# Kernel tuning notes

Hardware: AMD Instinct MI355X
Metric: run time of the kernel (lower is better)

Reference implementation:

```python
import jax, jax.numpy as jnp
import numpy as np

ZERO = 1e-8
L = 2            # num_gnn_layers
D = 256          # dim_node_features
B = 32           # graphs per batch
NPG = 256        # nodes per graph
N = B * NPG      # total nodes
E = 131072       # edges per edge-type
MAX_TOKENS = 256 # MAX_TOKENS_OF_A_POST
UPD = 0.5        # args.updated_weights_for_A


def _make_edges(k):
    k1, k2, k3 = jax.random.split(k, 3)
    g = jax.random.randint(k1, (E,), 0, B) * NPG          # keep edges within a graph
    src = g + jax.random.randint(k2, (E,), 0, NPG)
    dst = g + jax.random.randint(k3, (E,), 0, NPG)
    return jnp.stack([src, dst]).astype(jnp.int64)


def setup_inputs() -> dict:
    key = jax.random.key(0)
    ks = jax.random.split(key, 12)
    x = jax.random.normal(ks[0], (N, D), dtype=jnp.float32)
    ei_e = _make_edges(ks[1]); ew_e = jax.random.uniform(ks[2], (E,), dtype=jnp.float32)
    ei_p = _make_edges(ks[3]); ew_p = jax.random.uniform(ks[4], (E,), dtype=jnp.float32)
    ei_o = _make_edges(ks[5]); ew_o = jax.random.uniform(ks[6], (E,), dtype=jnp.float32)
    entity_mask = jax.random.randint(ks[7], (B, NPG), 0, 2).astype(bool)
    pattern_mask = jax.random.randint(ks[8], (B, NPG), 0, 2).astype(bool)
    s = 1.0 / np.sqrt(D)
    W_gcn = (jax.random.normal(ks[9], (L, 3, D, D), dtype=jnp.float32) * s)
    b_gcn = jnp.zeros((L, 3, D), dtype=jnp.float32)
    T_dyn = (jax.random.normal(ks[10], (L, D, D), dtype=jnp.float32) * s)
    return {
        'x': x,
        'edge_index_entity': ei_e, 'edge_weight_entity': ew_e,
        'edge_index_pattern': ei_p, 'edge_weight_pattern': ew_p,
        'edge_index_others': ei_o, 'edge_weight_others': ew_o,
        'entity_mask': entity_mask, 'pattern_mask': pattern_mask,
        'W_gcn': W_gcn, 'b_gcn': b_gcn, 'T_dyn': T_dyn,
    }


def _normalized_correlation_matrix(H):
    # cosine-similarity correlation matrix, symmetrically degree-normalized
    nrm = jnp.sqrt(jnp.sum(H * H, axis=1))
    A = (H @ H.T) / (nrm[:, None] * nrm[None, :] + ZERO)
    dinv = 1.0 / jnp.sqrt(jnp.abs(jnp.sum(A, axis=1)) + ZERO)
    return dinv[:, None] * A * dinv[None, :]


def _gcn(H, W, b, ei, ew):
    # GCNConv(add_self_loops=False, normalize=False): scatter-sum of weighted source messages
    msg = (H @ W)[ei[0]] * ew[:, None]                     # [E, D]
    return jax.ops.segment_sum(msg, ei[1], num_segments=N) + b


def _forward(x, we0, wp0, wo0, W_gcn, b_gcn, T_dyn,
             ei_e, ei_p, ei_o, entity_mask, pattern_mask):
    H = x
    A = _normalized_correlation_matrix(H)                  # [N, N]
    for i in range(L):
        if i == 0:
            we, wp, wo = we0, wp0, wo0
        else:
            # diag(one_hot(src) @ A @ one_hot(dst).T) == A[src, dst]
            we = A[ei_e[0], ei_e[1]]
            wp = A[ei_p[0], ei_p[1]]
            wo = A[ei_o[0], ei_o[1]]
        He = _gcn(H, W_gcn[i, 0], b_gcn[i, 0], ei_e, we)
        Hp = _gcn(H, W_gcn[i, 1], b_gcn[i, 1], ei_p, wp)
        Ho = _gcn(H, W_gcn[i, 2], b_gcn[i, 2], ei_o, wo)
        H = jax.nn.relu(He + Hp + Ho)
        A_hat = jax.nn.sigmoid((H @ T_dyn[i]) @ H.T)
        A = (1.0 - UPD) * A + UPD * A_hat
    # per-graph diagonal blocks of A  -> [B, NPG, NPG]
    A4 = A.reshape(B, NPG, B, NPG)
    idx = jnp.arange(B)
    blocks = A4[idx, :, idx, :]
    A_sum = jnp.sum(blocks, axis=-1)                       # [B, NPG]
    ent_cols = jnp.einsum('bij,bj->bi', blocks, entity_mask.astype(A.dtype))
    pat_cols = jnp.einsum('bij,bj->bi', blocks, pattern_mask.astype(A.dtype))
    map_pattern = A_sum - ent_cols
    map_entity = A_sum - pat_cols

    def finish(m):
        mn = jnp.min(m, axis=1, keepdims=True)
        mx = jnp.max(m, axis=1, keepdims=True)
        m = (m - mn) / (mx - mn + ZERO)
        m = m / (jnp.sum(m, axis=1, keepdims=True) + ZERO)
        return m[:, :MAX_TOKENS]                           # padding() with NPG==MAX_TOKENS

    return finish(map_entity), finish(map_pattern)


def reference(x, edge_index_entity, edge_weight_entity,
              edge_index_pattern, edge_weight_pattern,
              edge_index_others, edge_weight_others,
              entity_mask, pattern_mask, W_gcn, b_gcn, T_dyn):
    return _forward(x, edge_weight_entity, edge_weight_pattern, edge_weight_others,
                    W_gcn, b_gcn, T_dyn,
                    edge_index_entity, edge_index_pattern, edge_index_others,
                    entity_mask, pattern_mask)
```

## Files before the change

kernel.cpp:

```cpp
#include <hip/hip_runtime.h>

#define NND   8192
#define DDIM  256
#define NGRP  32
#define ZEROF 1e-8f
#define LSTR  40
#define TSTR  72
#define OFF_AH 0
#define OFF_AL 2560
#define OFF_BH 5120
#define OFF_BL 10240
#define OFF_TT 5120
#define LDS_U16 16384

typedef unsigned short u16;
typedef __attribute__((ext_vector_type(8))) short short8v;
typedef __attribute__((ext_vector_type(4))) float float4v;

__device__ inline u16 f2bf(float x) {
  unsigned u = __float_as_uint(x);
  u += 0x7fffu + ((u >> 16) & 1u);
  return (u16)(u >> 16);
}
__device__ inline float bf2f(u16 h) { return __uint_as_float((unsigned)h << 16); }
__device__ inline void split2(float x, u16& h, u16& l) {
  h = f2bf(x);
  l = f2bf(x - bf2f(h));
}

__device__ inline float wave_sum(float v) {
#pragma unroll
  for (int off = 32; off > 0; off >>= 1) v += __shfl_down(v, off, 64);
  return v;
}

#define LOAD_REGS(tt, kk)                                                                   \
  {                                                                                         \
    int m_ = tid >> 2, kq_ = (tid & 3) * 8;                                                 \
    size_t aoff_;                                                                           \
    if (MODE == 1)                                                                          \
      aoff_ = (size_t)((tt) * 256 + bym * 64 + m_) * 8192 + (size_t)(g * 256 + (kk) + kq_); \
    else if (MODE == 2 || MODE == 3)                                                        \
      aoff_ = (size_t)(g * 256 + bym * 64 + m_) * 256 + (kk) + kq_;                         \
    else                                                                                    \
      aoff_ = (size_t)(bym * 64 + m_) * 256 + (kk) + kq_;                                   \
    rAh = *(const short8v*)&Ah_g[aoff_];                                                    \
    rAl = *(const short8v*)&Al_g[aoff_];                                                    \
    size_t bbase_ = (MODE == 1) ? ((size_t)(g * 3 + (tt)) << 16)                            \
                  : ((MODE == 2 || MODE == 3) ? ((size_t)g << 16) : (size_t)0);             \
    if (HALF) {                                                                             \
      int n_ = tid & 63, kq2_ = (tid >> 6) * 8;                                             \
      size_t boff_ = bbase_ + (size_t)(col0 + n_) * 256 + (kk) + kq2_;                      \
      rBh0 = *(const short8v*)&Bh_g[boff_];                                                 \
      rBl0 = *(const short8v*)&Bl_g[boff_];                                                 \
    } else {                                                                                \
      int n_ = tid & 127, kq2_ = (tid >> 7) * 16;                                           \
      size_t boff_ = bbase_ + (size_t)(col0 + n_) * 256 + (kk) + kq2_;                      \
      rBh0 = *(const short8v*)&Bh_g[boff_]; rBh1 = *(const short8v*)&Bh_g[boff_ + 8];       \
      rBl0 = *(const short8v*)&Bl_g[boff_]; rBl1 = *(const short8v*)&Bl_g[boff_ + 8];       \
    }                                                                                       \
  }

template<int MODE, bool HALF>
__device__ __forceinline__ void mfma_body(
    u16* lds,
    const u16* __restrict__ Ah_g, const u16* __restrict__ Al_g,
    const u16* __restrict__ Bh_g, const u16* __restrict__ Bl_g,
    float* __restrict__ Cf, u16* __restrict__ Ch, u16* __restrict__ Cl,
    const float* __restrict__ nrm, const float* __restrict__ dinv,
    const float* __restrict__ bias,
    int bxm, int bym, int g) {
  u16* Ahs = lds + OFF_AH;
  u16* Als = lds + OFF_AL;
  u16* Bhs = lds + OFF_BH;
  u16* Bls = lds + OFF_BL;
  u16* Tt  = lds + OFF_TT;
  const int NJ = HALF ? 2 : 4;
  const int tid = threadIdx.x;
  const int col0 = bxm * (HALF ? 64 : 128);
  const int w = tid >> 6, lane = tid & 63;
  const int lm = lane & 15, lq = lane >> 4;
  const int wr = (w >> 1) * 32, wc = (w & 1) * (HALF ? 32 : 64);

  float4v acc[2][4];
#pragma unroll
  for (int i = 0; i < 2; ++i)
#pragma unroll
    for (int j = 0; j < NJ; ++j) acc[i][j] = (float4v)0.f;

  short8v rAh, rAl, rBh0, rBh1, rBl0, rBl1;
  const int TOTAL = (MODE == 1) ? 24 : 8;

  LOAD_REGS(0, 0);
  for (int step = 0; step < TOTAL; ++step) {
    if (step) __syncthreads();
    {
      int m = tid >> 2, kq = (tid & 3) * 8;
      *(short8v*)&Ahs[m * LSTR + kq] = rAh;
      *(short8v*)&Als[m * LSTR + kq] = rAl;
    }
    if (HALF) {
      int n = tid & 63, kq2 = (tid >> 6) * 8;
      *(short8v*)&Bhs[n * LSTR + kq2] = rBh0;
      *(short8v*)&Bls[n * LSTR + kq2] = rBl0;
    } else {
      int n = tid & 127, kq2 = (tid >> 7) * 16;
      *(short8v*)&Bhs[n * LSTR + kq2] = rBh0; *(short8v*)&Bhs[n * LSTR + kq2 + 8] = rBh1;
      *(short8v*)&Bls[n * LSTR + kq2] = rBl0; *(short8v*)&Bls[n * LSTR + kq2 + 8] = rBl1;
    }
    __syncthreads();
    int nxt = step + 1;
    if (nxt < TOTAL) {
      int tt = nxt >> 3, kk = (nxt & 7) * 32;
      LOAD_REGS(tt, kk);
    }
    short8v ah[2], al[2], bh[4], bl[4];
#pragma unroll
    for (int i = 0; i < 2; ++i) {
      int r = wr + i * 16 + lm;
      ah[i] = *(const short8v*)&Ahs[r * LSTR + lq * 8];
      al[i] = *(const short8v*)&Als[r * LSTR + lq * 8];
    }
#pragma unroll
    for (int j = 0; j < NJ; ++j) {
      int r = wc + j * 16 + lm;
      bh[j] = *(const short8v*)&Bhs[r * LSTR + lq * 8];
      bl[j] = *(const short8v*)&Bls[r * LSTR + lq * 8];
    }
#pragma unroll
    for (int i = 0; i < 2; ++i)
#pragma unroll
      for (int j = 0; j < NJ; ++j) {
        acc[i][j] = __builtin_amdgcn_mfma_f32_16x16x32_bf16(ah[i], bh[j], acc[i][j], 0, 0, 0);
        acc[i][j] = __builtin_amdgcn_mfma_f32_16x16x32_bf16(ah[i], bl[j], acc[i][j], 0, 0, 0);
        acc[i][j] = __builtin_amdgcn_mfma_f32_16x16x32_bf16(al[i], bh[j], acc[i][j], 0, 0, 0);
      }
  }

  if (MODE == 2 || MODE == 3) {
#pragma unroll
    for (int i = 0; i < 2; ++i) {
#pragma unroll
      for (int r = 0; r < 4; ++r) {
        int grow = g * 256 + bym * 64 + wr + i * 16 + lq * 4 + r;
        float di = 0.f, ni = 0.f;
        if (MODE == 2) { di = dinv[grow]; ni = nrm[grow]; }
#pragma unroll
        for (int j = 0; j < NJ; ++j) {
          int gcol = col0 + wc + j * 16 + lm;
          size_t ci = (size_t)grow * 256 + gcol;
          float v = acc[i][j][r];
          if (MODE == 2) {
            int gj = g * 256 + gcol;
            Cf[ci] = v * di * dinv[gj] / (ni * nrm[gj] + ZEROF);
          } else {
            Cf[ci] = 0.5f * Cf[ci] + 0.5f * (1.f / (1.f + expf(-v)));
          }
        }
      }
    }
  } else {
    float bsum[8];
    if (MODE == 1) {
#pragma unroll
      for (int i = 0; i < 2; ++i)
#pragma unroll
        for (int r = 0; r < 4; ++r) {
          int d = bym * 64 + wr + i * 16 + lq * 4 + r;
          bsum[i * 4 + r] = bias[d] + bias[256 + d] + bias[512 + d];
        }
    }
    u16 hv[32], lv[32];
#pragma unroll
    for (int i = 0; i < 2; ++i)
#pragma unroll
      for (int j = 0; j < NJ; ++j)
#pragma unroll
        for (int r = 0; r < 4; ++r) {
          float v = acc[i][j][r];
          if (MODE == 1) v = fmaxf(v + bsum[i * 4 + r], 0.f);
          split2(v, hv[(i * 4 + r) * NJ + j], lv[(i * 4 + r) * NJ + j]);
        }
    int ebase1 = (MODE == 1) ? (g * 256 + col0) : col0;
    int ebase2 = bym * 64;
    size_t estride = (MODE == 0) ? 8192 : 256;
#pragma unroll
    for (int ph = 0; ph < 2; ++ph) {
      __syncthreads();
      const u16* sv = ph ? lv : hv;
#pragma unroll
      for (int i = 0; i < 2; ++i)
#pragma unroll
        for (int j = 0; j < NJ; ++j)
#pragma unroll
          for (int r = 0; r < 4; ++r)
            Tt[(wc + j * 16 + lm) * TSTR + wr + i * 16 + lq * 4 + r] = sv[(i * 4 + r) * NJ + j];
      __syncthreads();
      u16* dst = ph ? Cl : Ch;
      int cc0 = tid >> 3, mm0 = (tid & 7) * 8;
#pragma unroll
      for (int it = 0; it < (HALF ? 2 : 4); ++it) {
        int cc = it * 32 + cc0;
        short8v v = *(const short8v*)&Tt[cc * TSTR + mm0];
        *(short8v*)&dst[(size_t)(ebase1 + cc) * estride + ebase2 + mm0] = v;
      }
    }
  }
}

__global__ void k_prep(const int* __restrict__ e0, const int* __restrict__ e1,
                       const int* __restrict__ e2, const unsigned char* __restrict__ m0,
                       const unsigned char* __restrict__ m1,
                       const float* __restrict__ W, const float* __restrict__ T,
                       const float* __restrict__ x,
                       const float* __restrict__ ew0, const float* __restrict__ ew1,
                       const float* __restrict__ ew2,
                       float* __restrict__ emf, float* __restrict__ pmf,
                       u16* __restrict__ Wth, u16* __restrict__ Wtl,
                       u16* __restrict__ sct, uint2* __restrict__ recs,
                       float* __restrict__ nrm, float* __restrict__ Spart,
                       u16* __restrict__ Hh, u16* __restrict__ Hl,
                       int E_, int nCvt, int nBkt) {
  __shared__ float tile[32][33];
  __shared__ float inv[64];
  __shared__ int nz[1];
  __shared__ unsigned int hcnt[768];
  __shared__ unsigned int hoff[768];
  __shared__ unsigned int ppart[256];
  __shared__ uint2 stage[768];
  const int b = blockIdx.x, tid = threadIdx.x;
  if (b < nCvt) {
    if (tid == 0) nz[0] = 0;
    __syncthreads();
    int i4 = tid * 4;
    int c = (m0[i4 + 1] != 0) + (m0[i4 + 2] != 0) + (m0[i4 + 3] != 0);
    if (c) atomicAdd(&nz[0], c);
    __syncthreads();
    int fM = (nz[0] == 0);
    int i = b * 256 + tid;
    if (i < NND) {
      unsigned char v = fM ? m0[4 * i] : m0[i];
      emf[i] = 1.f - (float)(v != 0);
    } else {
      int j = i - NND;
      unsigned char v = fM ? m1[4 * j] : m1[j];
      pmf[j] = 1.f - (float)(v != 0);
    }
  } else if (b < nCvt + nBkt) {
    if (tid == 0) nz[0] = 0;
    hcnt[tid] = 0; hcnt[tid + 256] = 0; hcnt[tid + 512] = 0;
    __syncthreads();
    if (e0[2 * tid + 1] != 0) atomicAdd(&nz[0], 1);
    __syncthreads();
    int fE = (nz[0] == 0);
    int e = (b - nCvt) * 256 + tid;
    bool valid = (e < E_);
    int mybid[3]; unsigned int myrec[3]; float myw[3];
    if (valid) {
#pragma unroll
      for (int t = 0; t < 3; ++t) {
        const int* ei = (t == 0) ? e0 : ((t == 1) ? e1 : e2);
        int src = fE ? ei[2 * e] : ei[e];
        int dst = fE ? ei[2 * (E_ + e)] : ei[E_ + e];
        int g = src >> 8, s = src & 255, d = dst & 255;
        mybid[t] = ((g * 3 + t) << 3) | (d >> 5);
        myrec[t] = (unsigned)(((d & 31) << 8) | s);
        myw[t] = (t == 0 ? ew0 : (t == 1 ? ew1 : ew2))[e];
        atomicAdd(&hcnt[mybid[t]], 1u);
      }
    }
    __syncthreads();
    unsigned c0 = hcnt[3 * tid], c1 = hcnt[3 * tid + 1], c2 = hcnt[3 * tid + 2];
    unsigned tsum = c0 + c1 + c2;
    ppart[tid] = tsum;
    __syncthreads();
    for (int off = 1; off < 256; off <<= 1) {
      unsigned v = (tid >= off) ? ppart[tid - off] : 0u;
      __syncthreads();
      ppart[tid] += v;
      __syncthreads();
    }
    unsigned base = ppart[tid] - tsum;
    hoff[3 * tid] = base;
    hoff[3 * tid + 1] = base + c0;
    hoff[3 * tid + 2] = base + c0 + c1;
    __syncthreads();
#pragma unroll
    for (int k = 0; k < 3; ++k) {
      int bin = tid + k * 256;
      unsigned cc = hcnt[bin]; if (cc > 31u) cc = 31u;
      sct[(size_t)(b - nCvt) * 768 + bin] = (u16)(hoff[bin] | (cc << 11));
    }
    __syncthreads();
    if (valid) {
#pragma unroll
      for (int t = 0; t < 3; ++t) {
        unsigned slot = atomicAdd(&hoff[mybid[t]], 1u);
        stage[slot] = make_uint2(myrec[t], __float_as_uint(myw[t]));
      }
    }
    __syncthreads();
    uint2* dstp = &recs[(size_t)(b - nCvt) * 768];
    dstp[tid] = stage[tid];
    dstp[tid + 256] = stage[tid + 256];
    dstp[tid + 512] = stage[tid + 512];
  } else if (b < nCvt + nBkt + 512) {
    int bb = b - nCvt - nBkt;
    int mat = bb >> 6, rem = bb & 63;
    int k0 = (rem >> 3) * 32, n0 = (rem & 7) * 32;
    const float* src = (mat < 6) ? (W + (size_t)mat * 65536) : (T + (size_t)(mat - 6) * 65536);
    int r = tid >> 3, c4 = (tid & 7) * 4;
    const float4 v = *(const float4*)&src[(size_t)(k0 + r) * 256 + n0 + c4];
    tile[r][c4 + 0] = v.x; tile[r][c4 + 1] = v.y; tile[r][c4 + 2] = v.z; tile[r][c4 + 3] = v.w;
    __syncthreads();
    float o[4] = {tile[c4 + 0][r], tile[c4 + 1][r], tile[c4 + 2][r], tile[c4 + 3][r]};
    u16 hh[4], ll[4];
#pragma unroll
    for (int q = 0; q < 4; ++q) split2(o[q], hh[q], ll[q]);
    size_t off = (size_t)mat * 65536 + (size_t)(n0 + r) * 256 + k0 + c4;
    *(ushort4*)&Wth[off] = *(ushort4*)hh;
    *(ushort4*)&Wtl[off] = *(ushort4*)ll;
  } else {
    int bn = b - nCvt - nBkt - 512;
    int n0 = bn * 64;
    int w = tid >> 6, lane = tid & 63;
    for (int it = 0; it < 16; ++it) {
      int nl = it * 4 + w;
      int node = n0 + nl;
      const float4 v = *(const float4*)&x[(size_t)node * 256 + lane * 4];
      u16 hh[4], ll[4];
      split2(v.x, hh[0], ll[0]); split2(v.y, hh[1], ll[1]);
      split2(v.z, hh[2], ll[2]); split2(v.w, hh[3], ll[3]);
      *(ushort4*)&Hh[(size_t)node * 256 + lane * 4] = *(ushort4*)hh;
      *(ushort4*)&Hl[(size_t)node * 256 + lane * 4] = *(ushort4*)ll;
      float s = wave_sum(v.x * v.x + v.y * v.y + v.z * v.z + v.w * v.w);
      if (lane == 0) { float nr = sqrtf(s); nrm[node] = nr; inv[nl] = 1.f / nr; }
    }
    __syncthreads();
    float s = 0.f;
    for (int i = 0; i < 64; ++i) s += x[(size_t)(n0 + i) * 256 + tid] * inv[i];
    Spart[bn * 256 + tid] = s;
  }
}

__global__ __launch_bounds__(256, 2) void k_gemmA(
    const u16* __restrict__ Hinh, const u16* __restrict__ Hinl,
    const u16* __restrict__ Wth, const u16* __restrict__ Wtl, int l,
    u16* __restrict__ XWTh, u16* __restrict__ XWTl) {
  __shared__ u16 lds[LDS_U16];
  const int b = blockIdx.x;
  mfma_body<0, false>(lds, Hinh, Hinl, Wth + (size_t)l * 768 * 256,
                      Wtl + (size_t)l * 768 * 256,
                      nullptr, XWTh, XWTl, nullptr, nullptr, nullptr,
                      b >> 7, b & 127, 0);
}

__global__ __launch_bounds__(256, 2) void k_mbuild(
    const u16* __restrict__ sct, const uint2* __restrict__ recs, int nBkt,
    const float* __restrict__ Abuf, u16* __restrict__ Mbh, u16* __restrict__ Mbl, int l,
    const float* __restrict__ x, const float* __restrict__ Spart,
    const float* __restrict__ nrm, float* __restrict__ dinv) {
  __shared__ float tile[8192];
  const int b = blockIdx.x, tid = threadIdx.x;
  if (b < 768) {
    int bid = b;
    int gt = bid >> 3, chunk = bid & 7;
    int g = gt / 3;
    float4 z = make_float4(0.f, 0.f, 0.f, 0.f);
#pragma unroll
    for (int k = 0; k < 8; ++k) ((float4*)tile)[k * 256 + tid] = z;
    __syncthreads();
    for (int bb = tid; bb < nBkt; bb += 256) {
      unsigned sc = sct[(size_t)bb * 768 + bid];
      unsigned start = sc & 2047u, cnt = sc >> 11;
      const uint2* rp = &recs[(size_t)bb * 768 + start];
      for (unsigned k = 0; k < cnt; ++k) {
        uint2 r = rp[k];
        int s = r.x & 255, d5 = (r.x >> 8) & 31;
        float w = l ? Abuf[(size_t)(g * 256 + s) * 256 + chunk * 32 + d5]
                    : __uint_as_float(r.y);
        atomicAdd(&tile[d5 * 256 + s], w);
      }
    }
    __syncthreads();
    size_t base4 = ((size_t)gt << 14) + ((size_t)chunk << 11);
#pragma unroll
    for (int k = 0; k < 8; ++k) {
      float4 f = ((float4*)tile)[k * 256 + tid];
      ushort4 h, lo;
      split2(f.x, h.x, lo.x); split2(f.y, h.y, lo.y);
      split2(f.z, h.z, lo.z); split2(f.w, h.w, lo.w);
      ((ushort4*)Mbh)[base4 + k * 256 + tid] = h;
      ((ushort4*)Mbl)[base4 + k * 256 + tid] = lo;
    }
  } else {
    float* Sl = tile;
    float s = 0.f;
    for (int bb = 0; bb < 128; ++bb) s += Spart[bb * 256 + tid];
    Sl[tid] = s;
    __syncthreads();
    int base = (b - 768) * 64;
    int w = tid >> 6, lane = tid & 63;
    const float4 sv = *(const float4*)&Sl[lane * 4];
    for (int it = 0; it < 16; ++it) {
      int node = base + it * 4 + w;
      const float4 v = *(const float4*)&x[(size_t)node * 256 + lane * 4];
      float s2 = wave_sum(v.x * sv.x + v.y * sv.y + v.z * sv.z + v.w * sv.w);
      if (lane == 0) {
        float rowsum = s2 / nrm[node];
        dinv[node] = rsqrtf(fabsf(rowsum) + ZEROF);
      }
    }
  }
}

__global__ __launch_bounds__(256, 2) void k_stageB(
    const u16* __restrict__ XWTh, const u16* __restrict__ XWTl,
    const u16* __restrict__ Mbh, const u16* __restrict__ Mbl,
    u16* __restrict__ Houth, u16* __restrict__ Houtl, const float* __restrict__ bias,
    const u16* __restrict__ xh, const u16* __restrict__ xl, float* __restrict__ Abuf,
    const float* __restrict__ nrm, const float* __restrict__ dinv) {
  __shared__ u16 lds[LDS_U16];
  const int b = blockIdx.x;
  if (b < 256) {
    int g = b & 31, r = b >> 5;
    mfma_body<1, false>(lds, XWTh, XWTl, Mbh, Mbl,
                        nullptr, Houth, Houtl, nullptr, nullptr, bias,
                        r & 1, r >> 1, g);
  } else {
    int bb = b - 256;
    int g = bb & 31, r = bb >> 5;
    mfma_body<2, true>(lds, xh, xl, xh, xl, Abuf, nullptr, nullptr,
                       nrm, dinv, nullptr, r >> 2, r & 3, g);
  }
}

__global__ __launch_bounds__(256, 2) void k_stageC(
    const u16* __restrict__ Wth, const u16* __restrict__ Wtl, int l,
    const u16* __restrict__ Hh, const u16* __restrict__ Hl,
    u16* __restrict__ tmph, u16* __restrict__ tmpl) {
  __shared__ u16 lds[LDS_U16];
  const int b = blockIdx.x;
  mfma_body<4, true>(lds, Wth + (size_t)(6 + l) * 65536, Wtl + (size_t)(6 + l) * 65536,
                     Hh, Hl, nullptr, tmph, tmpl, nullptr, nullptr, nullptr,
                     b & 127, b >> 7, 0);
}

__global__ __launch_bounds__(256, 2) void k_stageD(
    const u16* __restrict__ tmph, const u16* __restrict__ tmpl,
    const u16* __restrict__ Hh, const u16* __restrict__ Hl,
    float* __restrict__ Abuf) {
  __shared__ u16 lds[LDS_U16];
  const int b = blockIdx.x;
  int g = b & 31, r = b >> 5;
  mfma_body<3, true>(lds, tmph, tmpl, Hh, Hl, Abuf, nullptr, nullptr,
                     nullptr, nullptr, nullptr, r >> 2, r & 3, g);
}

__global__ void k_maps(const float* __restrict__ Abuf, const float* __restrict__ emf,
                       const float* __restrict__ pmf, float* __restrict__ out) {
  __shared__ float sme[256], smp[256], red[256];
  const int g = blockIdx.x, tid = threadIdx.x, w = tid >> 6, lane = tid & 63;
  const int j0 = g * 256 + lane * 4;
  const float4 pmv = *(const float4*)&pmf[j0];
  const float4 emv = *(const float4*)&emf[j0];
  for (int it = 0; it < 64; ++it) {
    int nl = it * 4 + w;
    const float4 a = *(const float4*)&Abuf[((size_t)g * 256 + nl) * 256 + lane * 4];
    float me = a.x * pmv.x + a.y * pmv.y + a.z * pmv.z + a.w * pmv.w;
    float mp = a.x * emv.x + a.y * emv.y + a.z * emv.z + a.w * emv.w;
#pragma unroll
    for (int off = 32; off > 0; off >>= 1) {
      me += __shfl_down(me, off, 64);
      mp += __shfl_down(mp, off, 64);
    }
    if (lane == 0) { sme[nl] = me; smp[nl] = mp; }
  }
  __syncthreads();
  for (int which = 0; which < 2; ++which) {
    float v = which ? smp[tid] : sme[tid];
    red[tid] = v; __syncthreads();
    for (int s = 128; s > 0; s >>= 1) { if (tid < s) red[tid] = fminf(red[tid], red[tid + s]); __syncthreads(); }
    float mn = red[0]; __syncthreads();
    red[tid] = v; __syncthreads();
    for (int s = 128; s > 0; s >>= 1) { if (tid < s) red[tid] = fmaxf(red[tid], red[tid + s]); __syncthreads(); }
    float mx = red[0]; __syncthreads();
    float m = (v - mn) / (mx - mn + ZEROF);
    red[tid] = m; __syncthreads();
    for (int s = 128; s > 0; s >>= 1) { if (tid < s) red[tid] += red[tid + s]; __syncthreads(); }
    float sum = red[0]; __syncthreads();
    out[which * NND + g * 256 + tid] = m / (sum + ZEROF);
  }
}

extern "C" void kernel_launch(void* const* d_in, const int* in_sizes, int n_in,
                              void* d_out, int out_size, void* d_ws, size_t ws_size,
                              hipStream_t stream) {
  const float* x = (const float*)d_in[0];
  const unsigned char* em_raw = (const unsigned char*)d_in[7];
  const unsigned char* pm_raw = (const unsigned char*)d_in[8];
  const float* W  = (const float*)d_in[9];
  const float* bg = (const float*)d_in[10];
  const float* T  = (const float*)d_in[11];
  float* out = (float*)d_out;
  const int E_ = in_sizes[2];

  const int nCvt = (2 * NND) / 256;
  const int nBkt = (E_ + 255) / 256;

  float* ws = (float*)d_ws;
  size_t o = 0;
  float* Abuf = ws + o; o += (size_t)NND * 256;
  u16* Mbh_l0 = (u16*)(ws + o); o += (size_t)NGRP * 3 * 65536 / 2;
  u16* Mbl_l0 = (u16*)(ws + o); o += (size_t)NGRP * 3 * 65536 / 2;
  u16* Mbh_l1 = (u16*)(ws + o); o += (size_t)NGRP * 3 * 65536 / 2;
  u16* Mbl_l1 = (u16*)(ws + o); o += (size_t)NGRP * 3 * 65536 / 2;
  u16* Hh   = (u16*)(ws + o); o += (size_t)NND * 256 / 2;
  u16* Hl   = (u16*)(ws + o); o += (size_t)NND * 256 / 2;
  u16* H2h  = (u16*)(ws + o); o += (size_t)NND * 256 / 2;
  u16* H2l  = (u16*)(ws + o); o += (size_t)NND * 256 / 2;
  u16* tmph = (u16*)(ws + o); o += (size_t)NND * 256 / 2;
  u16* tmpl = (u16*)(ws + o); o += (size_t)NND * 256 / 2;
  u16* XWTh = (u16*)(ws + o); o += (size_t)768 * NND / 2;
  u16* XWTl = (u16*)(ws + o); o += (size_t)768 * NND / 2;
  u16* Wth  = (u16*)(ws + o); o += (size_t)8 * 65536 / 2;
  u16* Wtl  = (u16*)(ws + o); o += (size_t)8 * 65536 / 2;
  float* nrm   = ws + o; o += NND;
  float* dinv  = ws + o; o += NND;
  float* Spart = ws + o; o += 128 * 256;
  float* emf   = ws + o; o += NND;
  float* pmf   = ws + o; o += NND;
  u16* sct     = (u16*)(ws + o); o += (size_t)nBkt * 768 / 2;
  uint2* recs  = (uint2*)(ws + o); o += (size_t)nBkt * 768 * 2;

  const float* ew0 = (const float*)d_in[2];
  const float* ew1 = (const float*)d_in[4];
  const float* ew2 = (const float*)d_in[6];

  k_prep<<<nCvt + nBkt + 512 + 128, 256, 0, stream>>>(
      (const int*)d_in[1], (const int*)d_in[3], (const int*)d_in[5], em_raw, pm_raw,
      W, T, x, ew0, ew1, ew2, emf, pmf, Wth, Wtl, sct, recs,
      nrm, Spart, Hh, Hl, E_, nCvt, nBkt);

  k_gemmA<<<768, 256, 0, stream>>>(Hh, Hl, Wth, Wtl, 0, XWTh, XWTl);
  k_mbuild<<<896, 256, 0, stream>>>(sct, recs, nBkt, Abuf, Mbh_l0, Mbl_l0, 0,
                                    x, Spart, nrm, dinv);
  k_stageB<<<768, 256, 0, stream>>>(XWTh, XWTl, Mbh_l0, Mbl_l0, H2h, H2l, bg,
                                    Hh, Hl, Abuf, nrm, dinv);
  k_stageC<<<512, 256, 0, stream>>>(Wth, Wtl, 0, H2h, H2l, tmph, tmpl);
  k_stageD<<<512, 256, 0, stream>>>(tmph, tmpl, H2h, H2l, Abuf);

  k_gemmA<<<768, 256, 0, stream>>>(H2h, H2l, Wth, Wtl, 1, XWTh, XWTl);
  k_mbuild<<<768, 256, 0, stream>>>(sct, recs, nBkt, Abuf, Mbh_l1, Mbl_l1, 1,
                                    x, Spart, nrm, dinv);
  k_stageB<<<256, 256, 0, stream>>>(XWTh, XWTl, Mbh_l1, Mbl_l1, Hh, Hl, bg + 768,
                                    nullptr, nullptr, nullptr, nullptr, nullptr);
  k_stageC<<<512, 256, 0, stream>>>(Wth, Wtl, 1, Hh, Hl, tmph, tmpl);
  k_stageD<<<512, 256, 0, stream>>>(tmph, tmpl, Hh, Hl, Abuf);

  k_maps<<<NGRP, 256, 0, stream>>>(Abuf, emf, pmf, out);
}
```

Before: 299.6 us.

## Merge independent kernels into combined launches to overlap GEMM and adjacency build

```diff
diff --git a/kernel.cpp b/kernel.cpp
--- a/kernel.cpp
+++ b/kernel.cpp
@@ -208,6 +208,42 @@
   }
 }
 
+__device__ __forceinline__ void mbuild_body(
+    float* tile, int bid, int l,
+    const u16* __restrict__ sct, const uint2* __restrict__ recs, int nBkt,
+    const float* __restrict__ Abuf, u16* __restrict__ Mbh, u16* __restrict__ Mbl) {
+  const int tid = threadIdx.x;
+  int gt = bid >> 3, chunk = bid & 7;
+  int g = gt / 3;
+  float4 z = make_float4(0.f, 0.f, 0.f, 0.f);
+#pragma unroll
+  for (int k = 0; k < 8; ++k) ((float4*)tile)[k * 256 + tid] = z;
+  __syncthreads();
+  for (int bb = tid; bb < nBkt; bb += 256) {
+    unsigned sc = sct[(size_t)bb * 768 + bid];
+    unsigned start = sc & 2047u, cnt = sc >> 11;
+    const uint2* rp = &recs[(size_t)bb * 768 + start];
+    for (unsigned k = 0; k < cnt; ++k) {
+      uint2 r = rp[k];
+      int s = r.x & 255, d5 = (r.x >> 8) & 31;
+      float w = l ? Abuf[(size_t)(g * 256 + s) * 256 + chunk * 32 + d5]
+                  : __uint_as_float(r.y);
+      atomicAdd(&tile[d5 * 256 + s], w);
+    }
+  }
+  __syncthreads();
+  size_t base4 = ((size_t)gt << 14) + ((size_t)chunk << 11);
+#pragma unroll
+  for (int k = 0; k < 8; ++k) {
+    float4 f = ((float4*)tile)[k * 256 + tid];
+    ushort4 h, lo;
+    split2(f.x, h.x, lo.x); split2(f.y, h.y, lo.y);
+    split2(f.z, h.z, lo.z); split2(f.w, h.w, lo.w);
+    ((ushort4*)Mbh)[base4 + k * 256 + tid] = h;
+    ((ushort4*)Mbl)[base4 + k * 256 + tid] = lo;
+  }
+}
+
 __global__ void k_prep(const int* __restrict__ e0, const int* __restrict__ e1,
                        const int* __restrict__ e2, const unsigned char* __restrict__ m0,
                        const unsigned char* __restrict__ m1,
@@ -343,63 +379,30 @@
   }
 }
 
-__global__ __launch_bounds__(256, 2) void k_gemmA(
+__global__ __launch_bounds__(256, 2) void k_stageA(
     const u16* __restrict__ Hinh, const u16* __restrict__ Hinl,
-    const u16* __restrict__ Wth, const u16* __restrict__ Wtl, int l,
-    u16* __restrict__ XWTh, u16* __restrict__ XWTl) {
+    const u16* __restrict__ Wth, const u16* __restrict__ Wtl,
+    u16* __restrict__ XWTh, u16* __restrict__ XWTl,
+    const u16* __restrict__ sct, const uint2* __restrict__ recs, int nBkt,
+    u16* __restrict__ Mbh, u16* __restrict__ Mbl,
+    const float* __restrict__ x, const float* __restrict__ Spart,
+    const float* __restrict__ nrm, float* __restrict__ dinv) {
   __shared__ u16 lds[LDS_U16];
   const int b = blockIdx.x;
-  mfma_body<0, false>(lds, Hinh, Hinl, Wth + (size_t)l * 768 * 256,
-                      Wtl + (size_t)l * 768 * 256,
-                      nullptr, XWTh, XWTl, nullptr, nullptr, nullptr,
-                      b >> 7, b & 127, 0);
-}
-
-__global__ __launch_bounds__(256, 2) void k_mbuild(
-    const u16* __restrict__ sct, const uint2* __restrict__ recs, int nBkt,
-    const float* __restrict__ Abuf, u16* __restrict__ Mbh, u16* __restrict__ Mbl, int l,
-    const float* __restrict__ x, const float* __restrict__ Spart,
-    const float* __restrict__ nrm, float* __restrict__ dinv) {
-  __shared__ float tile[8192];
-  const int b = blockIdx.x, tid = threadIdx.x;
   if (b < 768) {
-    int bid = b;
-    int gt = bid >> 3, chunk = bid & 7;
-    int g = gt / 3;
-    float4 z = make_float4(0.f, 0.f, 0.f, 0.f);
-#pragma unroll
-    for (int k = 0; k < 8; ++k) ((float4*)tile)[k * 256 + tid] = z;
-    __syncthreads();
-    for (int bb = tid; bb < nBkt; bb += 256) {
-      unsigned sc = sct[(size_t)bb * 768 + bid];
-      unsigned start = sc & 2047u, cnt = sc >> 11;
-      const uint2* rp = &recs[(size_t)bb * 768 + start];
-      for (unsigned k = 0; k < cnt; ++k) {
-        uint2 r = rp[k];
-        int s = r.x & 255, d5 = (r.x >> 8) & 31;
-        float w = l ? Abuf[(size_t)(g * 256 + s) * 256 + chunk * 32 + d5]
-                    : __uint_as_float(r.y);
-        atomicAdd(&tile[d5 * 256 + s], w);
-      }
-    }
-    __syncthreads();
-    size_t base4 = ((size_t)gt << 14) + ((size_t)chunk << 11);
-#pragma unroll
-    for (int k = 0; k < 8; ++k) {
-      float4 f = ((float4*)tile)[k * 256 + tid];
-      ushort4 h, lo;
-      split2(f.x, h.x, lo.x); split2(f.y, h.y, lo.y);
-      split2(f.z, h.z, lo.z); split2(f.w, h.w, lo.w);
-      ((ushort4*)Mbh)[base4 + k * 256 + tid] = h;
-      ((ushort4*)Mbl)[base4 + k * 256 + tid] = lo;
-    }
+    mfma_body<0, false>(lds, Hinh, Hinl, Wth, Wtl,
+                        nullptr, XWTh, XWTl, nullptr, nullptr, nullptr,
+                        b >> 7, b & 127, 0);
+  } else if (b < 1536) {
+    mbuild_body((float*)lds, b - 768, 0, sct, recs, nBkt, nullptr, Mbh, Mbl);
   } else {
-    float* Sl = tile;
+    float* Sl = (float*)lds;
+    const int tid = threadIdx.x;
     float s = 0.f;
     for (int bb = 0; bb < 128; ++bb) s += Spart[bb * 256 + tid];
     Sl[tid] = s;
     __syncthreads();
-    int base = (b - 768) * 64;
+    int base = (b - 1536) * 64;
     int w = tid >> 6, lane = tid & 63;
     const float4 sv = *(const float4*)&Sl[lane * 4];
     for (int it = 0; it < 16; ++it) {
@@ -412,6 +415,13 @@
       }
     }
   }
+}
+
+__global__ __launch_bounds__(256, 2) void k_mbuild(
+    const u16* __restrict__ sct, const uint2* __restrict__ recs, int nBkt,
+    const float* __restrict__ Abuf, u16* __restrict__ Mbh, u16* __restrict__ Mbl) {
+  __shared__ float tile[8192];
+  mbuild_body(tile, blockIdx.x, 1, sct, recs, nBkt, Abuf, Mbh, Mbl);
 }
 
 __global__ __launch_bounds__(256, 2) void k_stageB(
@@ -432,6 +442,25 @@
     int g = bb & 31, r = bb >> 5;
     mfma_body<2, true>(lds, xh, xl, xh, xl, Abuf, nullptr, nullptr,
                        nrm, dinv, nullptr, r >> 2, r & 3, g);
+  }
+}
+
+__global__ __launch_bounds__(256, 2) void k_stageCA(
+    const u16* __restrict__ Wth, const u16* __restrict__ Wtl,
+    const u16* __restrict__ H2h, const u16* __restrict__ H2l,
+    u16* __restrict__ tmph, u16* __restrict__ tmpl,
+    u16* __restrict__ XWTh, u16* __restrict__ XWTl) {
+  __shared__ u16 lds[LDS_U16];
+  const int b = blockIdx.x;
+  if (b < 512) {
+    mfma_body<4, true>(lds, Wth + (size_t)6 * 65536, Wtl + (size_t)6 * 65536,
+                       H2h, H2l, nullptr, tmph, tmpl, nullptr, nullptr, nullptr,
+                       b & 127, b >> 7, 0);
+  } else {
+    int bb = b - 512;
+    mfma_body<0, false>(lds, H2h, H2l, Wth + (size_t)768 * 256, Wtl + (size_t)768 * 256,
+                        nullptr, XWTh, XWTl, nullptr, nullptr, nullptr,
+                        bb >> 7, bb & 127, 0);
   }
 }
 
@@ -542,17 +571,15 @@
       W, T, x, ew0, ew1, ew2, emf, pmf, Wth, Wtl, sct, recs,
       nrm, Spart, Hh, Hl, E_, nCvt, nBkt);
 
-  k_gemmA<<<768, 256, 0, stream>>>(Hh, Hl, Wth, Wtl, 0, XWTh, XWTl);
-  k_mbuild<<<896, 256, 0, stream>>>(sct, recs, nBkt, Abuf, Mbh_l0, Mbl_l0, 0,
-                                    x, Spart, nrm, dinv);
+  k_stageA<<<1664, 256, 0, stream>>>(Hh, Hl, Wth, Wtl, XWTh, XWTl,
+                                     sct, recs, nBkt, Mbh_l0, Mbl_l0,
+                                     x, Spart, nrm, dinv);
   k_stageB<<<768, 256, 0, stream>>>(XWTh, XWTl, Mbh_l0, Mbl_l0, H2h, H2l, bg,
                                     Hh, Hl, Abuf, nrm, dinv);
-  k_stageC<<<512, 256, 0, stream>>>(Wth, Wtl, 0, H2h, H2l, tmph, tmpl);
+  k_stageCA<<<1280, 256, 0, stream>>>(Wth, Wtl, H2h, H2l, tmph, tmpl, XWTh, XWTl);
   k_stageD<<<512, 256, 0, stream>>>(tmph, tmpl, H2h, H2l, Abuf);
 
-  k_gemmA<<<768, 256, 0, stream>>>(H2h, H2l, Wth, Wtl, 1, XWTh, XWTl);
-  k_mbuild<<<768, 256, 0, stream>>>(sct, recs, nBkt, Abuf, Mbh_l1, Mbl_l1, 1,
-                                    x, Spart, nrm, dinv);
+  k_mbuild<<<768, 256, 0, stream>>>(sct, recs, nBkt, Abuf, Mbh_l1, Mbl_l1);
   k_stageB<<<256, 256, 0, stream>>>(XWTh, XWTl, Mbh_l1, Mbl_l1, Hh, Hl, bg + 768,
                                     nullptr, nullptr, nullptr, nullptr, nullptr);
   k_stageC<<<512, 256, 0, stream>>>(Wth, Wtl, 1, Hh, Hl, tmph, tmpl);
```

Result: no change. 296.5 us (-1.0%).
